# Kernel optimization log

Measured on AMD Instinct MI355X. Metric: run time of the kernel, lower is better.

Reference implementation:

```python
import jax, jax.numpy as jnp
import numpy as np

B, T, D, H = 32, 2048, 512, 512


def setup_inputs() -> dict:
    key = jax.random.key(0)
    ks = jax.random.split(key, 16)
    s_x = 1.0 / np.sqrt(D)
    s_h = 1.0 / np.sqrt(H)
    return {
        "x": jax.random.normal(ks[0], (B, T, D), dtype=jnp.float32),
        "Wxi": jax.random.normal(ks[1], (D, H), dtype=jnp.float32) * s_x,
        "Whi": jax.random.normal(ks[2], (H, H), dtype=jnp.float32) * s_h,
        "bi": jax.random.normal(ks[3], (H,), dtype=jnp.float32) * 0.01,
        "Wxf": jax.random.normal(ks[4], (D, H), dtype=jnp.float32) * s_x,
        "Whf": jax.random.normal(ks[5], (H, H), dtype=jnp.float32) * s_h,
        "bf": jax.random.normal(ks[6], (H,), dtype=jnp.float32) * 0.01,
        "Wxo": jax.random.normal(ks[7], (D, H), dtype=jnp.float32) * s_x,
        "Who": jax.random.normal(ks[8], (H, H), dtype=jnp.float32) * s_h,
        "bo": jax.random.normal(ks[9], (H,), dtype=jnp.float32) * 0.01,
        "Wxc": jax.random.normal(ks[10], (D, H), dtype=jnp.float32) * s_x,
        "Whc": jax.random.normal(ks[11], (H, H), dtype=jnp.float32) * s_h,
        "bc": jax.random.normal(ks[12], (H,), dtype=jnp.float32) * 0.01,
        "Wd": jax.random.normal(ks[13], (H, 1), dtype=jnp.float32) * s_h,
        "bd": jnp.zeros((1,), dtype=jnp.float32),
    }


def _lstm(x, Wxi, Whi, bi, Wxf, Whf, bf, Wxo, Who, bo, Wxc, Whc, bc):
    # Precompute input projections for all timesteps in one batched GEMM each.
    # Shapes: [B, T, H] -> transpose to time-major [T, B, H] for scan.
    xi = (jnp.einsum('btd,dh->bth', x, Wxi) + bi).transpose(1, 0, 2)
    xf = (jnp.einsum('btd,dh->bth', x, Wxf) + bf).transpose(1, 0, 2)
    xo = (jnp.einsum('btd,dh->bth', x, Wxo) + bo).transpose(1, 0, 2)
    xc = (jnp.einsum('btd,dh->bth', x, Wxc) + bc).transpose(1, 0, 2)

    h0 = jnp.zeros((x.shape[0], Whi.shape[0]), dtype=x.dtype)
    c0 = jnp.zeros_like(h0)

    def step(carry, gates_t):
        h, c = carry
        gi, gf, go, gc = gates_t
        I = jax.nn.sigmoid(gi + h @ Whi)
        F = jax.nn.sigmoid(gf + h @ Whf)
        O = jax.nn.sigmoid(go + h @ Who)
        Ct = jnp.tanh(gc + h @ Whc)
        c_new = F * c + I * Ct
        h_new = O * jnp.tanh(c_new)
        return (h_new, c_new), h_new

    _, hs = jax.lax.scan(step, (h0, c0), (xi, xf, xo, xc))
    return hs.transpose(1, 0, 2)  # [B, T, H]


def reference(x, Wxi, Whi, bi, Wxf, Whf, bf, Wxo, Who, bo, Wxc, Whc, bc, Wd, bd):
    hs = _lstm(x, Wxi, Whi, bi, Wxf, Whf, bf, Wxo, Who, bo, Wxc, Whc, bc)
    return jnp.einsum('bth,ho->bto', hs, Wd) + bd  # [B, T, 1]
```

## Files before the change

kernel.cpp:

```cpp
#include <hip/hip_runtime.h>
#include <cstdint>
#include <cstddef>

#define B_  32
#define T_  2048
#define D_  512
#define H_  512
#define NWG 32

typedef unsigned int   u32;
typedef unsigned short u16;
typedef u32   u32x4  __attribute__((ext_vector_type(4)));
typedef u32   u32x2  __attribute__((ext_vector_type(2)));
typedef float f32x4  __attribute__((ext_vector_type(4)));
typedef __bf16 bf16x8 __attribute__((ext_vector_type(8)));

__device__ __forceinline__ u16 f2bf(float f) {
  u32 u = __builtin_bit_cast(u32, f);
  u32 r = (u + 0x7fffu + ((u >> 16) & 1u)) >> 16;
  return (u16)r;
}
__device__ __forceinline__ f32x4 g4_from_bf(u32x2 p) {
  f32x4 r;
  r[0] = __builtin_bit_cast(float, (p[0] & 0xffffu) << 16);
  r[1] = __builtin_bit_cast(float, (p[0] & 0xffff0000u));
  r[2] = __builtin_bit_cast(float, (p[1] & 0xffffu) << 16);
  r[3] = __builtin_bit_cast(float, (p[1] & 0xffff0000u));
  return r;
}
__device__ __forceinline__ float sigm(float x) {
  return __builtin_amdgcn_rcpf(1.0f + __expf(-x));
}
__device__ __forceinline__ float tanh_fast(float x) {
  return 1.0f - 2.0f * __builtin_amdgcn_rcpf(__expf(2.0f * x) + 1.0f);
}

__global__ __launch_bounds__(256) void k_cast_x(const float* __restrict__ x,
                                                u16* __restrict__ xb) {
  long i = (long)blockIdx.x * 256 + threadIdx.x;
  int  dc = (int)(i & 63);
  long m  = i >> 6;
  int  t  = (int)(m >> 5), b = (int)(m & 31);
  const float* src = x + ((long)b * T_ + t) * D_ + (dc << 3);
  f32x4 a = *(const f32x4*)(src);
  f32x4 c = *(const f32x4*)(src + 4);
  u32x4 pv;
  pv[0] = (u32)f2bf(a[0]) | ((u32)f2bf(a[1]) << 16);
  pv[1] = (u32)f2bf(a[2]) | ((u32)f2bf(a[3]) << 16);
  pv[2] = (u32)f2bf(c[0]) | ((u32)f2bf(c[1]) << 16);
  pv[3] = (u32)f2bf(c[2]) | ((u32)f2bf(c[3]) << 16);
  *(u32x4*)(xb + (m << 9) + (dc << 3)) = pv;
}

__global__ __launch_bounds__(256) void k_pack_w(
    const float* __restrict__ Wxi, const float* __restrict__ Whi, const float* __restrict__ bi,
    const float* __restrict__ Wxf, const float* __restrict__ Whf, const float* __restrict__ bfv,
    const float* __restrict__ Wxo, const float* __restrict__ Who, const float* __restrict__ bo,
    const float* __restrict__ Wxc, const float* __restrict__ Whc, const float* __restrict__ bc,
    u16* __restrict__ w4xt, u16* __restrict__ w4ht, float* __restrict__ bias4) {
  int blk = blockIdx.x, tid = threadIdx.x;
  if (blk == 1024) {
    for (int i = tid; i < 2048; i += 256) {
      int hcol = i >> 2, g = i & 3;
      const float* bsrc = (g == 0 ? bi : g == 1 ? bfv : g == 2 ? bo : bc);
      bias4[i] = bsrc[hcol];
    }
    return;
  }
  bool isx = (blk < 512);
  long s = (long)(isx ? blk : blk - 512) * 256 + tid;
  int n = (int)(s >> 6);
  int c = (int)(s & 63);
  int hcol = n >> 2, g = n & 3;
  const float* W = isx ? (g == 0 ? Wxi : g == 1 ? Wxf : g == 2 ? Wxo : Wxc)
                       : (g == 0 ? Whi : g == 1 ? Whf : g == 2 ? Who : Whc);
  u16* dst = (isx ? w4xt : w4ht) + ((long)n << 9) + (c << 3);
#pragma unroll
  for (int j = 0; j < 8; j++) dst[j] = f2bf(W[(long)((c << 3) + j) * H_ + hcol]);
}

template <int G32>
__global__ __launch_bounds__(256) void k_gemm(const u16* __restrict__ xb,
                                              const u16* __restrict__ w4xt,
                                              const float* __restrict__ bias4,
                                              char* __restrict__ gates0) {
  __shared__ __align__(16) unsigned char As[128 * 32 * 2];
  __shared__ __align__(16) unsigned char Bs[128 * 32 * 2];
  int tid = threadIdx.x;
  int bm = blockIdx.x & 511;
  int bn = blockIdx.x >> 9;
  long m0 = (long)bm << 7;
  int  n0 = bn << 7;
  int wv = tid >> 6, lane = tid & 63;
  int wr = wv >> 1, wc = wv & 1;
  int lr = lane & 15, lc = lane >> 4;

  f32x4 acc[4][4];
#pragma unroll
  for (int i = 0; i < 4; i++)
#pragma unroll
    for (int j = 0; j < 4; j++) acc[i][j] = (f32x4){0.f, 0.f, 0.f, 0.f};

  for (int kt = 0; kt < 16; kt++) {
#pragma unroll
    for (int h = 0; h < 2; h++) {
      int s = h * 256 + tid;
      int row = s >> 2, ch = s & 3;
      u32x4 va = *(const u32x4*)(xb + ((m0 + row) << 9) + (kt << 5) + (ch << 3));
      *(u32x4*)(As + (((row << 6) + (ch << 4)) ^ ((row & 3) << 4))) = va;
      u32x4 vb = *(const u32x4*)(w4xt + (((long)n0 + row) << 9) + (kt << 5) + (ch << 3));
      *(u32x4*)(Bs + (((row << 6) + (ch << 4)) ^ ((row & 3) << 4))) = vb;
    }
    __syncthreads();
    bf16x8 af[4], bfr[4];
#pragma unroll
    for (int mi = 0; mi < 4; mi++) {
      int row = (wr << 6) + (mi << 4) + lr;
      af[mi] = __builtin_bit_cast(bf16x8,
          *(const u32x4*)(As + (((row << 6) + (lc << 4)) ^ ((row & 3) << 4))));
    }
#pragma unroll
    for (int ni = 0; ni < 4; ni++) {
      int row = (wc << 6) + (ni << 4) + lr;
      bfr[ni] = __builtin_bit_cast(bf16x8,
          *(const u32x4*)(Bs + (((row << 6) + (lc << 4)) ^ ((row & 3) << 4))));
    }
#pragma unroll
    for (int mi = 0; mi < 4; mi++)
#pragma unroll
      for (int ni = 0; ni < 4; ni++)
        acc[mi][ni] = __builtin_amdgcn_mfma_f32_16x16x32_bf16(af[mi], bfr[ni], acc[mi][ni], 0, 0, 0);
    __syncthreads();
  }
#pragma unroll
  for (int mi = 0; mi < 4; mi++) {
#pragma unroll
    for (int ni = 0; ni < 4; ni++) {
      int col = n0 + (wc << 6) + (ni << 4) + lr;
      float bias = bias4[col];
#pragma unroll
      for (int r = 0; r < 4; r++) {
        long row = m0 + (wr << 6) + (mi << 4) + (lc << 2) + r;
        float v = acc[mi][ni][r] + bias;
        if constexpr (G32) ((float*)gates0)[(row << 11) + col] = v;
        else               ((u16*)gates0)[(row << 11) + col] = f2bf(v);
      }
    }
  }
}

template <int G32>
__global__ __launch_bounds__(256, 1) void k_rnn(const u16* __restrict__ w4ht,
                                                const char* __restrict__ gates0,
                                                const float* __restrict__ wd,
                                                u16* __restrict__ h_buf,
                                                float* __restrict__ po,
                                                u32* __restrict__ flags) {
  __shared__ __align__(16) float G_all[32 * 64];
  __shared__ float hn_s[32 * 16];
  __shared__ float wd_s[16];

  const int tid = threadIdx.x;
  const int w = blockIdx.x;
  const int wv = tid >> 6, lane = tid & 63;
  const int lr = lane & 15, lc = lane >> 4;
  const int hhalf = wv >> 1;
  const int wcol  = wv & 1;
  const int ncol0 = (wcol << 5) + lr;
  const int ncol1 = ncol0 + 16;

  u32x4 wfr0[16], wfr1[16];
  {
    const u16* wb = w4ht + ((long)(w << 6) << 9);
#pragma unroll
    for (int kk = 0; kk < 16; kk++) {
      wfr0[kk] = *(const u32x4*)(wb + ((long)ncol0 << 9) + (kk << 5) + (lc << 3));
      wfr1[kk] = *(const u32x4*)(wb + ((long)ncol1 << 9) + (kk << 5) + (lc << 3));
    }
  }
  if (tid < 16) wd_s[tid] = wd[(w << 4) + tid];
  __syncthreads();

  const int pb = tid >> 4;
  const int jj = tid & 15;
  float c0 = 0.f, c1 = 0.f;

  const int arow = (hhalf << 4) + lr;
  const u32 hbase = (u32)(arow << 10);
  const u32 poll_off = (u32)((lane & 31) << 6);
  const u32 flag_off = (u32)(w << 6);
  const u32 st0 = (u32)((((pb) << 9) + (w << 4) + jj) << 1);
  const u32 st1 = (u32)((((pb + 16) << 9) + (w << 4) + jj) << 1);

#pragma unroll 1
  for (int t = 0; t < T_; t++) {
    const u16* hb_cur = h_buf + ((t & 1) << 14);
    u16* hb_nxt = h_buf + (((t + 1) & 1) << 14);

    f32x4 gfa, gfb; u32x2 gba, gbb;
    {
      long i0 = ((long)t * 32 + pb) * 2048 + (w << 6) + (jj << 2);
      long i1 = i0 + 16 * 2048;
      if constexpr (G32) {
        gfa = *(const f32x4*)((const float*)gates0 + i0);
        gfb = *(const f32x4*)((const float*)gates0 + i1);
      } else {
        gba = *(const u32x2*)((const u16*)gates0 + i0);
        gbb = *(const u32x2*)((const u16*)gates0 + i1);
      }
    }

    if (t > 0) {
      u32 fv;
      do {
        asm volatile("global_load_dword %0, %1, %2 sc1\n\ts_waitcnt vmcnt(0)"
                     : "=v"(fv) : "v"(poll_off), "s"(flags) : "memory");
      } while (!__all(fv >= (u32)t));
    }

    u32x4 ha[16];
#pragma unroll
    for (int kk = 0; kk < 16; kk++) {
      asm volatile("global_load_dwordx4 %0, %1, %2 sc1"
                   : "=v"(ha[kk]) : "v"(hbase + (u32)(kk << 6) + (u32)(lc << 4)),
                     "s"(hb_cur));
    }
    asm volatile("s_waitcnt vmcnt(0)" ::: "memory");
    __builtin_amdgcn_sched_barrier(0);

    f32x4 acc0 = {0.f, 0.f, 0.f, 0.f}, acc1 = {0.f, 0.f, 0.f, 0.f};
#pragma unroll
    for (int kk = 0; kk < 16; kk++) {
      bf16x8 a = __builtin_bit_cast(bf16x8, ha[kk]);
      acc0 = __builtin_amdgcn_mfma_f32_16x16x32_bf16(a, __builtin_bit_cast(bf16x8, wfr0[kk]), acc0, 0, 0, 0);
      acc1 = __builtin_amdgcn_mfma_f32_16x16x32_bf16(a, __builtin_bit_cast(bf16x8, wfr1[kk]), acc1, 0, 0, 0);
    }
#pragma unroll
    for (int r = 0; r < 4; r++) {
      int grow = (hhalf << 4) + (lc << 2) + r;
      G_all[(grow << 6) + ncol0] = acc0[r];
      G_all[(grow << 6) + ncol1] = acc1[r];
    }
    __syncthreads();

    {
      f32x4 g0a, g0b;
      if constexpr (G32) { g0a = gfa; g0b = gfb; }
      else { g0a = g4_from_bf(gba); g0b = g4_from_bf(gbb); }

      f32x4 gv = *(const f32x4*)(&G_all[(pb << 6) + (jj << 2)]);
      float I = sigm(gv[0] + g0a[0]);
      float F = sigm(gv[1] + g0a[1]);
      float O = sigm(gv[2] + g0a[2]);
      float Ct = tanh_fast(gv[3] + g0a[3]);
      float cn = F * c0 + I * Ct;
      float hn = O * tanh_fast(cn);
      c0 = cn;
      hn_s[(pb << 4) + jj] = hn;
      u32 hv0 = (u32)f2bf(hn);
      asm volatile("global_store_short %0, %1, %2 sc1"
                   :: "v"(st0), "v"(hv0), "s"(hb_nxt) : "memory");

      f32x4 gw = *(const f32x4*)(&G_all[((pb + 16) << 6) + (jj << 2)]);
      float I2 = sigm(gw[0] + g0b[0]);
      float F2 = sigm(gw[1] + g0b[1]);
      float O2 = sigm(gw[2] + g0b[2]);
      float Ct2 = tanh_fast(gw[3] + g0b[3]);
      float cn2 = F2 * c1 + I2 * Ct2;
      float hn2 = O2 * tanh_fast(cn2);
      c1 = cn2;
      hn_s[((pb + 16) << 4) + jj] = hn2;
      u32 hv1 = (u32)f2bf(hn2);
      asm volatile("global_store_short %0, %1, %2 sc1"
                   :: "v"(st1), "v"(hv1), "s"(hb_nxt) : "memory");
    }

    asm volatile("s_waitcnt vmcnt(0)" ::: "memory");
    __syncthreads();
    if (tid == 0) {
      u32 fval = (u32)(t + 1);
      asm volatile("global_store_dword %0, %1, %2 sc1"
                   :: "v"(flag_off), "v"(fval), "s"(flags) : "memory");
    }

    if (tid < 32) {
      float s = 0.f;
#pragma unroll
      for (int j = 0; j < 16; j++) s += hn_s[(tid << 4) + j] * wd_s[j];
      po[((long)t * NWG + w) * 32 + tid] = s;
    }
  }
}

__global__ __launch_bounds__(256) void k_reduce(const float* __restrict__ po,
                                                const float* __restrict__ bd,
                                                float* __restrict__ out) {
  int tid = threadIdx.x;
  int b = tid & 31, tl = tid >> 5;
  int t = blockIdx.x * 8 + tl;
  float s = bd[0];
#pragma unroll
  for (int w = 0; w < NWG; w++) s += po[((long)t * NWG + w) * 32 + b];
  out[(long)b * T_ + t] = s;
}

extern "C" void kernel_launch(void* const* d_in, const int* in_sizes, int n_in,
                              void* d_out, int out_size, void* d_ws, size_t ws_size,
                              hipStream_t stream) {
  const float* x   = (const float*)d_in[0];
  const float* Wxi = (const float*)d_in[1];
  const float* Whi = (const float*)d_in[2];
  const float* bi  = (const float*)d_in[3];
  const float* Wxf = (const float*)d_in[4];
  const float* Whf = (const float*)d_in[5];
  const float* bfv = (const float*)d_in[6];
  const float* Wxo = (const float*)d_in[7];
  const float* Who = (const float*)d_in[8];
  const float* bo  = (const float*)d_in[9];
  const float* Wxc = (const float*)d_in[10];
  const float* Whc = (const float*)d_in[11];
  const float* bc  = (const float*)d_in[12];
  const float* Wd  = (const float*)d_in[13];
  const float* bd  = (const float*)d_in[14];

  char* ws = (char*)d_ws;
  constexpr size_t OFF_FLAGS = 0;
  constexpr size_t OFF_HBUF  = 2048;
  constexpr size_t OFF_PO    = OFF_HBUF + 65536;
  constexpr size_t OFF_XB    = OFF_PO + 8388608;
  constexpr size_t OFF_W4XT  = OFF_XB + 67108864;
  constexpr size_t OFF_W4HT  = OFF_W4XT + 2097152;
  constexpr size_t OFF_BIAS  = OFF_W4HT + 2097152;
  constexpr size_t OFF_G0    = OFF_BIAS + 8192;
  constexpr size_t TOT_F32   = OFF_G0 + (size_t)65536 * 2048 * 4;
  bool g32 = (ws_size >= TOT_F32);

  u32* flags     = (u32*)(ws + OFF_FLAGS);
  u16* h_buf     = (u16*)(ws + OFF_HBUF);
  float* po      = (float*)(ws + OFF_PO);
  u16* xb        = (u16*)(ws + OFF_XB);
  u16* w4xt      = (u16*)(ws + OFF_W4XT);
  u16* w4ht      = (u16*)(ws + OFF_W4HT);
  float* bias4   = (float*)(ws + OFF_BIAS);
  char* gates0   = ws + OFF_G0;

  hipMemsetAsync(d_ws, 0, OFF_PO, stream);

  k_cast_x<<<16384, 256, 0, stream>>>(x, xb);
  k_pack_w<<<1025, 256, 0, stream>>>(Wxi, Whi, bi, Wxf, Whf, bfv, Wxo, Who, bo,
                                     Wxc, Whc, bc, w4xt, w4ht, bias4);
  if (g32) {
    k_gemm<1><<<8192, 256, 0, stream>>>(xb, w4xt, bias4, gates0);
    k_rnn<1><<<NWG, 256, 0, stream>>>(w4ht, gates0, Wd, h_buf, po, flags);
  } else {
    k_gemm<0><<<8192, 256, 0, stream>>>(xb, w4xt, bias4, gates0);
    k_rnn<0><<<NWG, 256, 0, stream>>>(w4ht, gates0, Wd, h_buf, po, flags);
  }
  k_reduce<<<256, 256, 0, stream>>>(po, bd, (float*)d_out);
}
```

Baseline: 9.061 ms.

## Remove per-step block barriers: per-wave flags, LDS weights, prefetched gate inputs

The recurrent kernel now stages each workgroup's slice of the recurrent weights in swizzled LDS. Each wave computes all 32 batch rows for its own 4 hidden columns, so gates stay in registers and the per-step LDS exchange and both __syncthreads disappear. Each wave publishes its own flag, pollers read two flags per lane, the next step's input gates are prefetched during the current step, and the output dot-product partials are reduced with shuffles into a four-times-larger partial buffer. This targets the intra-block barrier latency on the serial critical path, at the cost of 128 flags to poll, extra LDS weight reads per step, and a larger final reduction.

Measured after the change: 17.41 ms. 1.92x slower.

```diff
diff --git a/kernel.cpp b/kernel.cpp
--- a/kernel.cpp
+++ b/kernel.cpp
@@ -156,139 +156,169 @@
                                                 u16* __restrict__ h_buf,
                                                 float* __restrict__ po,
                                                 u32* __restrict__ flags) {
-  __shared__ __align__(16) float G_all[32 * 64];
-  __shared__ float hn_s[32 * 16];
-  __shared__ float wd_s[16];
+  __shared__ __align__(16) unsigned char whs[64 * 1024];
 
   const int tid = threadIdx.x;
   const int w = blockIdx.x;
   const int wv = tid >> 6, lane = tid & 63;
   const int lr = lane & 15, lc = lane >> 4;
-  const int hhalf = wv >> 1;
-  const int wcol  = wv & 1;
-  const int ncol0 = (wcol << 5) + lr;
-  const int ncol1 = ncol0 + 16;
-
-  u32x4 wfr0[16], wfr1[16];
-  {
-    const u16* wb = w4ht + ((long)(w << 6) << 9);
-#pragma unroll
-    for (int kk = 0; kk < 16; kk++) {
-      wfr0[kk] = *(const u32x4*)(wb + ((long)ncol0 << 9) + (kk << 5) + (lc << 3));
-      wfr1[kk] = *(const u32x4*)(wb + ((long)ncol1 << 9) + (kk << 5) + (lc << 3));
-    }
-  }
-  if (tid < 16) wd_s[tid] = wd[(w << 4) + tid];
+
+#pragma unroll 4
+  for (int i = 0; i < 16; i++) {
+    int s = i * 256 + tid;
+    int n = s >> 6, c = s & 63;
+    u32x4 v = *(const u32x4*)(w4ht + ((long)((w << 6) + n) << 9) + (c << 3));
+    *(u32x4*)(whs + (((n << 10) + (c << 4)) ^ ((n & 7) << 4))) = v;
+  }
   __syncthreads();
 
-  const int pb = tid >> 4;
-  const int jj = tid & 15;
+  const int mycol = (w << 4) + (wv << 2) + lc;
+  const float wdr = wd[mycol];
   float c0 = 0.f, c1 = 0.f;
 
-  const int arow = (hhalf << 4) + lr;
-  const u32 hbase = (u32)(arow << 10);
-  const u32 poll_off = (u32)((lane & 31) << 6);
-  const u32 flag_off = (u32)(w << 6);
-  const u32 st0 = (u32)((((pb) << 9) + (w << 4) + jj) << 1);
-  const u32 st1 = (u32)((((pb + 16) << 9) + (w << 4) + jj) << 1);
+  const u32 hoff = (u32)((lr << 10) + (lc << 4));
+  const u32 st0 = (u32)(((lr << 9) + mycol) << 1);
+  const u32 st1 = (u32)((((lr + 16) << 9) + mycol) << 1);
+  const u32 poll_off = (u32)(lane << 3);
+  const u32 flag_off = (u32)(((w << 2) + wv) << 2);
+
+  const int sh = G32 ? 2 : 1;
+  u32 go = (u32)(((lr << 11) + (mycol << 2)) << sh);
+  const u32 gstep = 65536u << sh;
+  const u32 gdel  = 32768u << sh;
+
+  u32x4 gfa, gfb, gna, gnb;
+  u32x2 g2a, g2b, g2na, g2nb;
+  if constexpr (G32) {
+    asm volatile("global_load_dwordx4 %0, %1, %2" : "=v"(gfa) : "v"(go), "s"(gates0));
+    asm volatile("global_load_dwordx4 %0, %1, %2" : "=v"(gfb) : "v"(go + gdel), "s"(gates0));
+  } else {
+    asm volatile("global_load_dwordx2 %0, %1, %2" : "=v"(g2a) : "v"(go), "s"(gates0));
+    asm volatile("global_load_dwordx2 %0, %1, %2" : "=v"(g2b) : "v"(go + gdel), "s"(gates0));
+  }
+
+  const u32 wrow  = (u32)((wv << 4) + lr);
+  const u32 wbase = wrow << 10;
+  const u32 wswz  = (wrow & 7) << 4;
 
 #pragma unroll 1
   for (int t = 0; t < T_; t++) {
     const u16* hb_cur = h_buf + ((t & 1) << 14);
     u16* hb_nxt = h_buf + (((t + 1) & 1) << 14);
 
-    f32x4 gfa, gfb; u32x2 gba, gbb;
-    {
-      long i0 = ((long)t * 32 + pb) * 2048 + (w << 6) + (jj << 2);
-      long i1 = i0 + 16 * 2048;
-      if constexpr (G32) {
-        gfa = *(const f32x4*)((const float*)gates0 + i0);
-        gfb = *(const f32x4*)((const float*)gates0 + i1);
-      } else {
-        gba = *(const u32x2*)((const u16*)gates0 + i0);
-        gbb = *(const u32x2*)((const u16*)gates0 + i1);
-      }
-    }
-
     if (t > 0) {
-      u32 fv;
+      u32x2 fv;
       do {
-        asm volatile("global_load_dword %0, %1, %2 sc1\n\ts_waitcnt vmcnt(0)"
+        asm volatile("global_load_dwordx2 %0, %1, %2 sc1\n\ts_waitcnt vmcnt(0)"
                      : "=v"(fv) : "v"(poll_off), "s"(flags) : "memory");
-      } while (!__all(fv >= (u32)t));
-    }
-
-    u32x4 ha[16];
+      } while (!__all((fv[0] >= (u32)t) && (fv[1] >= (u32)t)));
+    }
+
+    u32x4 hlo[16], hhi[16];
 #pragma unroll
     for (int kk = 0; kk < 16; kk++) {
       asm volatile("global_load_dwordx4 %0, %1, %2 sc1"
-                   : "=v"(ha[kk]) : "v"(hbase + (u32)(kk << 6) + (u32)(lc << 4)),
-                     "s"(hb_cur));
+                   : "=v"(hlo[kk]) : "v"(hoff + (u32)(kk << 6)), "s"(hb_cur));
+      asm volatile("global_load_dwordx4 %0, %1, %2 sc1"
+                   : "=v"(hhi[kk]) : "v"(hoff + (u32)(kk << 6) + 16384u), "s"(hb_cur));
+    }
+
+    f32x4 aL0 = {0.f,0.f,0.f,0.f}, aL1 = {0.f,0.f,0.f,0.f};
+    f32x4 aH0 = {0.f,0.f,0.f,0.f}, aH1 = {0.f,0.f,0.f,0.f};
+    asm volatile("s_waitcnt vmcnt(16)" ::: "memory");
+    __builtin_amdgcn_sched_barrier(0);
+#pragma unroll
+    for (int kk = 0; kk < 8; kk++) {
+      bf16x8 aw = __builtin_bit_cast(bf16x8,
+          *(const u32x4*)(whs + ((wbase + (u32)((kk << 6) + (lc << 4))) ^ wswz)));
+      bf16x8 bl = __builtin_bit_cast(bf16x8, hlo[kk]);
+      bf16x8 bh = __builtin_bit_cast(bf16x8, hhi[kk]);
+      if (kk & 1) {
+        aL1 = __builtin_amdgcn_mfma_f32_16x16x32_bf16(aw, bl, aL1, 0, 0, 0);
+        aH1 = __builtin_amdgcn_mfma_f32_16x16x32_bf16(aw, bh, aH1, 0, 0, 0);
+      } else {
+        aL0 = __builtin_amdgcn_mfma_f32_16x16x32_bf16(aw, bl, aL0, 0, 0, 0);
+        aH0 = __builtin_amdgcn_mfma_f32_16x16x32_bf16(aw, bh, aH0, 0, 0, 0);
+      }
     }
     asm volatile("s_waitcnt vmcnt(0)" ::: "memory");
     __builtin_amdgcn_sched_barrier(0);
-
-    f32x4 acc0 = {0.f, 0.f, 0.f, 0.f}, acc1 = {0.f, 0.f, 0.f, 0.f};
-#pragma unroll
-    for (int kk = 0; kk < 16; kk++) {
-      bf16x8 a = __builtin_bit_cast(bf16x8, ha[kk]);
-      acc0 = __builtin_amdgcn_mfma_f32_16x16x32_bf16(a, __builtin_bit_cast(bf16x8, wfr0[kk]), acc0, 0, 0, 0);
-      acc1 = __builtin_amdgcn_mfma_f32_16x16x32_bf16(a, __builtin_bit_cast(bf16x8, wfr1[kk]), acc1, 0, 0, 0);
-    }
-#pragma unroll
-    for (int r = 0; r < 4; r++) {
-      int grow = (hhalf << 4) + (lc << 2) + r;
-      G_all[(grow << 6) + ncol0] = acc0[r];
-      G_all[(grow << 6) + ncol1] = acc1[r];
-    }
-    __syncthreads();
-
-    {
-      f32x4 g0a, g0b;
-      if constexpr (G32) { g0a = gfa; g0b = gfb; }
-      else { g0a = g4_from_bf(gba); g0b = g4_from_bf(gbb); }
-
-      f32x4 gv = *(const f32x4*)(&G_all[(pb << 6) + (jj << 2)]);
-      float I = sigm(gv[0] + g0a[0]);
-      float F = sigm(gv[1] + g0a[1]);
-      float O = sigm(gv[2] + g0a[2]);
-      float Ct = tanh_fast(gv[3] + g0a[3]);
-      float cn = F * c0 + I * Ct;
-      float hn = O * tanh_fast(cn);
-      c0 = cn;
-      hn_s[(pb << 4) + jj] = hn;
-      u32 hv0 = (u32)f2bf(hn);
-      asm volatile("global_store_short %0, %1, %2 sc1"
-                   :: "v"(st0), "v"(hv0), "s"(hb_nxt) : "memory");
-
-      f32x4 gw = *(const f32x4*)(&G_all[((pb + 16) << 6) + (jj << 2)]);
-      float I2 = sigm(gw[0] + g0b[0]);
-      float F2 = sigm(gw[1] + g0b[1]);
-      float O2 = sigm(gw[2] + g0b[2]);
-      float Ct2 = tanh_fast(gw[3] + g0b[3]);
-      float cn2 = F2 * c1 + I2 * Ct2;
-      float hn2 = O2 * tanh_fast(cn2);
-      c1 = cn2;
-      hn_s[((pb + 16) << 4) + jj] = hn2;
-      u32 hv1 = (u32)f2bf(hn2);
-      asm volatile("global_store_short %0, %1, %2 sc1"
-                   :: "v"(st1), "v"(hv1), "s"(hb_nxt) : "memory");
-    }
-
-    asm volatile("s_waitcnt vmcnt(0)" ::: "memory");
-    __syncthreads();
-    if (tid == 0) {
+#pragma unroll
+    for (int kk = 8; kk < 16; kk++) {
+      bf16x8 aw = __builtin_bit_cast(bf16x8,
+          *(const u32x4*)(whs + ((wbase + (u32)((kk << 6) + (lc << 4))) ^ wswz)));
+      bf16x8 bl = __builtin_bit_cast(bf16x8, hlo[kk]);
+      bf16x8 bh = __builtin_bit_cast(bf16x8, hhi[kk]);
+      if (kk & 1) {
+        aL1 = __builtin_amdgcn_mfma_f32_16x16x32_bf16(aw, bl, aL1, 0, 0, 0);
+        aH1 = __builtin_amdgcn_mfma_f32_16x16x32_bf16(aw, bh, aH1, 0, 0, 0);
+      } else {
+        aL0 = __builtin_amdgcn_mfma_f32_16x16x32_bf16(aw, bl, aL0, 0, 0, 0);
+        aH0 = __builtin_amdgcn_mfma_f32_16x16x32_bf16(aw, bh, aH0, 0, 0, 0);
+      }
+    }
+    f32x4 GL = aL0 + aL1, GH = aH0 + aH1;
+
+    f32x4 g0a, g0b;
+    if constexpr (G32) {
+      g0a = __builtin_bit_cast(f32x4, gfa);
+      g0b = __builtin_bit_cast(f32x4, gfb);
+    } else {
+      g0a = g4_from_bf(g2a);
+      g0b = g4_from_bf(g2b);
+    }
+
+    float I  = sigm(GL[0] + g0a[0]);
+    float F  = sigm(GL[1] + g0a[1]);
+    float O  = sigm(GL[2] + g0a[2]);
+    float Ct = tanh_fast(GL[3] + g0a[3]);
+    float cn = F * c0 + I * Ct;
+    float hn = O * tanh_fast(cn);
+    c0 = cn;
+    u32 hv0 = (u32)f2bf(hn);
+    asm volatile("global_store_short %0, %1, %2 sc1"
+                 :: "v"(st0), "v"(hv0), "s"(hb_nxt) : "memory");
+
+    float I2  = sigm(GH[0] + g0b[0]);
+    float F2  = sigm(GH[1] + g0b[1]);
+    float O2  = sigm(GH[2] + g0b[2]);
+    float Ct2 = tanh_fast(GH[3] + g0b[3]);
+    float cn2 = F2 * c1 + I2 * Ct2;
+    float hn2 = O2 * tanh_fast(cn2);
+    c1 = cn2;
+    u32 hv1 = (u32)f2bf(hn2);
+    asm volatile("global_store_short %0, %1, %2 sc1"
+                 :: "v"(st1), "v"(hv1), "s"(hb_nxt) : "memory");
+
+    u32 gq = (t + 1 < T_) ? (go + gstep) : go;
+    if constexpr (G32) {
+      asm volatile("global_load_dwordx4 %0, %1, %2" : "=v"(gna) : "v"(gq), "s"(gates0));
+      asm volatile("global_load_dwordx4 %0, %1, %2" : "=v"(gnb) : "v"(gq + gdel), "s"(gates0));
+    } else {
+      asm volatile("global_load_dwordx2 %0, %1, %2" : "=v"(g2na) : "v"(gq), "s"(gates0));
+      asm volatile("global_load_dwordx2 %0, %1, %2" : "=v"(g2nb) : "v"(gq + gdel), "s"(gates0));
+    }
+    go = gq;
+
+    asm volatile("s_waitcnt vmcnt(2)" ::: "memory");
+    __builtin_amdgcn_sched_barrier(0);
+    if (lane == 0) {
       u32 fval = (u32)(t + 1);
       asm volatile("global_store_dword %0, %1, %2 sc1"
                    :: "v"(flag_off), "v"(fval), "s"(flags) : "memory");
     }
 
-    if (tid < 32) {
-      float s = 0.f;
-#pragma unroll
-      for (int j = 0; j < 16; j++) s += hn_s[(tid << 4) + j] * wd_s[j];
-      po[((long)t * NWG + w) * 32 + tid] = s;
-    }
+    float p0 = hn * wdr, p1 = hn2 * wdr;
+    p0 += __shfl_xor(p0, 16); p0 += __shfl_xor(p0, 32);
+    p1 += __shfl_xor(p1, 16); p1 += __shfl_xor(p1, 32);
+    if (lc == 0) {
+      float* pp = po + ((long)t * 128 + (w << 2) + wv) * 32;
+      pp[lr] = p0;
+      pp[lr + 16] = p1;
+    }
+
+    if constexpr (G32) { gfa = gna; gfb = gnb; }
+    else               { g2a = g2na; g2b = g2nb; }
   }
 }
 
@@ -299,8 +329,8 @@
   int b = tid & 31, tl = tid >> 5;
   int t = blockIdx.x * 8 + tl;
   float s = bd[0];
-#pragma unroll
-  for (int w = 0; w < NWG; w++) s += po[((long)t * NWG + w) * 32 + b];
+#pragma unroll 8
+  for (int w = 0; w < 128; w++) s += po[((long)t * 128 + w) * 32 + b];
   out[(long)b * T_ + t] = s;
 }
 
@@ -325,9 +355,9 @@
 
   char* ws = (char*)d_ws;
   constexpr size_t OFF_FLAGS = 0;
-  constexpr size_t OFF_HBUF  = 2048;
+  constexpr size_t OFF_HBUF  = 1024;
   constexpr size_t OFF_PO    = OFF_HBUF + 65536;
-  constexpr size_t OFF_XB    = OFF_PO + 8388608;
+  constexpr size_t OFF_XB    = OFF_PO + 33554432;
   constexpr size_t OFF_W4XT  = OFF_XB + 67108864;
   constexpr size_t OFF_W4HT  = OFF_W4XT + 2097152;
   constexpr size_t OFF_BIAS  = OFF_W4HT + 2097152;
@@ -344,7 +374,7 @@
   float* bias4   = (float*)(ws + OFF_BIAS);
   char* gates0   = ws + OFF_G0;
 
-  hipMemsetAsync(d_ws, 0, OFF_PO, stream);
+  hipMemsetAsync(d_ws, 0, OFF_HBUF + 65536, stream);
 
   k_cast_x<<<16384, 256, 0, stream>>>(x, xb);
   k_pack_w<<<1025, 256, 0, stream>>>(Wxi, Whi, bi, Wxf, Whf, bfv, Wxo, Who, bo,
```

## Move recurrent weights to swizzled LDS, use per-wave flags and shuffle-reduce output

Applied to the files above, without the earlier changes.

The recurrent weight fragments now live in a 64KB XOR-swizzled LDS buffer instead of 32 u32x4 registers per thread, which frees VGPRs at the cost of two LDS reads per MFMA. The end-of-step __syncthreads before publishing the flag is removed: each wave writes its own flag, and wave 0 polls all 128 per-wave flags with dwordx2 loads before a block barrier. The dense-output partial dot product moves from a 32-thread LDS loop to a shuffle-xor reduction across the 16 lanes. Together these target the per-step barrier and serial tail latency in the persistent recurrent loop, but add LDS traffic on the critical path and a wider flag poll.

Result: slower. 11.36 ms (+25.3%).

```diff
diff --git a/kernel.cpp b/kernel.cpp
--- a/kernel.cpp
+++ b/kernel.cpp
@@ -156,9 +156,8 @@
                                                 u16* __restrict__ h_buf,
                                                 float* __restrict__ po,
                                                 u32* __restrict__ flags) {
+  __shared__ __align__(16) unsigned char whs[64 * 1024];
   __shared__ __align__(16) float G_all[32 * 64];
-  __shared__ float hn_s[32 * 16];
-  __shared__ float wd_s[16];
 
   const int tid = threadIdx.x;
   const int w = blockIdx.x;
@@ -169,33 +168,43 @@
   const int ncol0 = (wcol << 5) + lr;
   const int ncol1 = ncol0 + 16;
 
-  u32x4 wfr0[16], wfr1[16];
-  {
-    const u16* wb = w4ht + ((long)(w << 6) << 9);
-#pragma unroll
-    for (int kk = 0; kk < 16; kk++) {
-      wfr0[kk] = *(const u32x4*)(wb + ((long)ncol0 << 9) + (kk << 5) + (lc << 3));
-      wfr1[kk] = *(const u32x4*)(wb + ((long)ncol1 << 9) + (kk << 5) + (lc << 3));
-    }
-  }
-  if (tid < 16) wd_s[tid] = wd[(w << 4) + tid];
+#pragma unroll 4
+  for (int i = 0; i < 16; i++) {
+    int s = i * 256 + tid;
+    int n = s >> 6, c = s & 63;
+    u32x4 v = *(const u32x4*)(w4ht + ((long)((w << 6) + n) << 9) + (c << 3));
+    *(u32x4*)(whs + (((n << 10) + (c << 4)) ^ ((n & 7) << 4))) = v;
+  }
   __syncthreads();
 
   const int pb = tid >> 4;
   const int jj = tid & 15;
   float c0 = 0.f, c1 = 0.f;
-
-  const int arow = (hhalf << 4) + lr;
-  const u32 hbase = (u32)(arow << 10);
-  const u32 poll_off = (u32)((lane & 31) << 6);
-  const u32 flag_off = (u32)(w << 6);
+  const float wdr = wd[(w << 4) + jj];
+
+  const u32 hbase = (u32)(((hhalf << 4) + lr) << 10);
+  const u32 poll_off = (u32)(lane << 3);
+  const u32 flag_off = (u32)(((w << 2) + wv) << 2);
   const u32 st0 = (u32)((((pb) << 9) + (w << 4) + jj) << 1);
   const u32 st1 = (u32)((((pb + 16) << 9) + (w << 4) + jj) << 1);
+  const u32 b0base = (u32)(ncol0 << 10), b0swz = (u32)((ncol0 & 7) << 4);
+  const u32 b1base = (u32)(ncol1 << 10), b1swz = (u32)((ncol1 & 7) << 4);
 
 #pragma unroll 1
   for (int t = 0; t < T_; t++) {
     const u16* hb_cur = h_buf + ((t & 1) << 14);
     u16* hb_nxt = h_buf + (((t + 1) & 1) << 14);
+
+    if (t > 0) {
+      if (wv == 0) {
+        u32x2 fv;
+        do {
+          asm volatile("global_load_dwordx2 %0, %1, %2 sc1\n\ts_waitcnt vmcnt(0)"
+                       : "=v"(fv) : "v"(poll_off), "s"(flags) : "memory");
+        } while (!__all((fv[0] >= (u32)t) && (fv[1] >= (u32)t)));
+      }
+      __syncthreads();
+    }
 
     f32x4 gfa, gfb; u32x2 gba, gbb;
     {
@@ -210,14 +219,6 @@
       }
     }
 
-    if (t > 0) {
-      u32 fv;
-      do {
-        asm volatile("global_load_dword %0, %1, %2 sc1\n\ts_waitcnt vmcnt(0)"
-                     : "=v"(fv) : "v"(poll_off), "s"(flags) : "memory");
-      } while (!__all(fv >= (u32)t));
-    }
-
     u32x4 ha[16];
 #pragma unroll
     for (int kk = 0; kk < 16; kk++) {
@@ -228,12 +229,15 @@
     asm volatile("s_waitcnt vmcnt(0)" ::: "memory");
     __builtin_amdgcn_sched_barrier(0);
 
-    f32x4 acc0 = {0.f, 0.f, 0.f, 0.f}, acc1 = {0.f, 0.f, 0.f, 0.f};
+    f32x4 acc0 = {0.f,0.f,0.f,0.f}, acc1 = {0.f,0.f,0.f,0.f};
 #pragma unroll
     for (int kk = 0; kk < 16; kk++) {
-      bf16x8 a = __builtin_bit_cast(bf16x8, ha[kk]);
-      acc0 = __builtin_amdgcn_mfma_f32_16x16x32_bf16(a, __builtin_bit_cast(bf16x8, wfr0[kk]), acc0, 0, 0, 0);
-      acc1 = __builtin_amdgcn_mfma_f32_16x16x32_bf16(a, __builtin_bit_cast(bf16x8, wfr1[kk]), acc1, 0, 0, 0);
+      u32 ko = (u32)((kk << 6) + (lc << 4));
+      bf16x8 a  = __builtin_bit_cast(bf16x8, ha[kk]);
+      bf16x8 b0 = __builtin_bit_cast(bf16x8, *(const u32x4*)(whs + ((b0base + ko) ^ b0swz)));
+      bf16x8 b1 = __builtin_bit_cast(bf16x8, *(const u32x4*)(whs + ((b1base + ko) ^ b1swz)));
+      acc0 = __builtin_amdgcn_mfma_f32_16x16x32_bf16(a, b0, acc0, 0, 0, 0);
+      acc1 = __builtin_amdgcn_mfma_f32_16x16x32_bf16(a, b1, acc1, 0, 0, 0);
     }
 #pragma unroll
     for (int r = 0; r < 4; r++) {
@@ -243,6 +247,7 @@
     }
     __syncthreads();
 
+    float hnA, hnB;
     {
       f32x4 g0a, g0b;
       if constexpr (G32) { g0a = gfa; g0b = gfb; }
@@ -254,10 +259,9 @@
       float O = sigm(gv[2] + g0a[2]);
       float Ct = tanh_fast(gv[3] + g0a[3]);
       float cn = F * c0 + I * Ct;
-      float hn = O * tanh_fast(cn);
+      hnA = O * tanh_fast(cn);
       c0 = cn;
-      hn_s[(pb << 4) + jj] = hn;
-      u32 hv0 = (u32)f2bf(hn);
+      u32 hv0 = (u32)f2bf(hnA);
       asm volatile("global_store_short %0, %1, %2 sc1"
                    :: "v"(st0), "v"(hv0), "s"(hb_nxt) : "memory");
 
@@ -267,27 +271,30 @@
       float O2 = sigm(gw[2] + g0b[2]);
       float Ct2 = tanh_fast(gw[3] + g0b[3]);
       float cn2 = F2 * c1 + I2 * Ct2;
-      float hn2 = O2 * tanh_fast(cn2);
+      hnB = O2 * tanh_fast(cn2);
       c1 = cn2;
-      hn_s[((pb + 16) << 4) + jj] = hn2;
-      u32 hv1 = (u32)f2bf(hn2);
+      u32 hv1 = (u32)f2bf(hnB);
       asm volatile("global_store_short %0, %1, %2 sc1"
                    :: "v"(st1), "v"(hv1), "s"(hb_nxt) : "memory");
     }
 
     asm volatile("s_waitcnt vmcnt(0)" ::: "memory");
-    __syncthreads();
-    if (tid == 0) {
+    __builtin_amdgcn_sched_barrier(0);
+    if (lane == 0) {
       u32 fval = (u32)(t + 1);
       asm volatile("global_store_dword %0, %1, %2 sc1"
                    :: "v"(flag_off), "v"(fval), "s"(flags) : "memory");
     }
 
-    if (tid < 32) {
-      float s = 0.f;
-#pragma unroll
-      for (int j = 0; j < 16; j++) s += hn_s[(tid << 4) + j] * wd_s[j];
-      po[((long)t * NWG + w) * 32 + tid] = s;
+    float pA = hnA * wdr, pB = hnB * wdr;
+    pA += __shfl_xor(pA, 1); pA += __shfl_xor(pA, 2);
+    pA += __shfl_xor(pA, 4); pA += __shfl_xor(pA, 8);
+    pB += __shfl_xor(pB, 1); pB += __shfl_xor(pB, 2);
+    pB += __shfl_xor(pB, 4); pB += __shfl_xor(pB, 8);
+    if (jj == 0) {
+      float* pp = po + ((long)t * NWG + w) * 32;
+      pp[pb] = pA;
+      pp[pb + 16] = pB;
     }
   }
 }
```

## Prefetch flag poll early and compute output projection with wave shuffles

Applied to the files above, without the earlier changes.

Issues the flag load for the next step right after publishing this step's flag, so the poll latency overlaps the output-projection work. On the next iteration the spin loop is skipped if the prefetched value already meets the target. The output dot product with Wd now uses in-register xor-shuffle reductions instead of a shared-memory staging array read by 32 threads, removing the hn_s/wd_s LDS traffic and one setup barrier. The prefetched flag can still be stale, in which case the old polling path runs as a fallback.

After: 9.170 ms. About the same (+1.2%).

```diff
diff --git a/kernel.cpp b/kernel.cpp
--- a/kernel.cpp
+++ b/kernel.cpp
@@ -157,8 +157,6 @@
                                                 float* __restrict__ po,
                                                 u32* __restrict__ flags) {
   __shared__ __align__(16) float G_all[32 * 64];
-  __shared__ float hn_s[32 * 16];
-  __shared__ float wd_s[16];
 
   const int tid = threadIdx.x;
   const int w = blockIdx.x;
@@ -178,12 +176,11 @@
       wfr1[kk] = *(const u32x4*)(wb + ((long)ncol1 << 9) + (kk << 5) + (lc << 3));
     }
   }
-  if (tid < 16) wd_s[tid] = wd[(w << 4) + tid];
-  __syncthreads();
 
   const int pb = tid >> 4;
   const int jj = tid & 15;
   float c0 = 0.f, c1 = 0.f;
+  const float wdr = wd[(w << 4) + jj];
 
   const int arow = (hhalf << 4) + lr;
   const u32 hbase = (u32)(arow << 10);
@@ -191,6 +188,8 @@
   const u32 flag_off = (u32)(w << 6);
   const u32 st0 = (u32)((((pb) << 9) + (w << 4) + jj) << 1);
   const u32 st1 = (u32)((((pb + 16) << 9) + (w << 4) + jj) << 1);
+
+  u32 fpre = 0;
 
 #pragma unroll 1
   for (int t = 0; t < T_; t++) {
@@ -211,11 +210,14 @@
     }
 
     if (t > 0) {
-      u32 fv;
-      do {
-        asm volatile("global_load_dword %0, %1, %2 sc1\n\ts_waitcnt vmcnt(0)"
-                     : "=v"(fv) : "v"(poll_off), "s"(flags) : "memory");
-      } while (!__all(fv >= (u32)t));
+      asm volatile("s_waitcnt vmcnt(0)" ::: "memory");
+      if (!__all(fpre >= (u32)t)) {
+        u32 fv;
+        do {
+          asm volatile("global_load_dword %0, %1, %2 sc1\n\ts_waitcnt vmcnt(0)"
+                       : "=v"(fv) : "v"(poll_off), "s"(flags) : "memory");
+        } while (!__all(fv >= (u32)t));
+      }
     }
 
     u32x4 ha[16];
@@ -243,6 +245,7 @@
     }
     __syncthreads();
 
+    float hnA, hnB;
     {
       f32x4 g0a, g0b;
       if constexpr (G32) { g0a = gfa; g0b = gfb; }
@@ -254,10 +257,9 @@
       float O = sigm(gv[2] + g0a[2]);
       float Ct = tanh_fast(gv[3] + g0a[3]);
       float cn = F * c0 + I * Ct;
-      float hn = O * tanh_fast(cn);
+      hnA = O * tanh_fast(cn);
       c0 = cn;
-      hn_s[(pb << 4) + jj] = hn;
-      u32 hv0 = (u32)f2bf(hn);
+      u32 hv0 = (u32)f2bf(hnA);
       asm volatile("global_store_short %0, %1, %2 sc1"
                    :: "v"(st0), "v"(hv0), "s"(hb_nxt) : "memory");
 
@@ -267,10 +269,9 @@
       float O2 = sigm(gw[2] + g0b[2]);
       float Ct2 = tanh_fast(gw[3] + g0b[3]);
       float cn2 = F2 * c1 + I2 * Ct2;
-      float hn2 = O2 * tanh_fast(cn2);
+      hnB = O2 * tanh_fast(cn2);
       c1 = cn2;
-      hn_s[((pb + 16) << 4) + jj] = hn2;
-      u32 hv1 = (u32)f2bf(hn2);
+      u32 hv1 = (u32)f2bf(hnB);
       asm volatile("global_store_short %0, %1, %2 sc1"
                    :: "v"(st1), "v"(hv1), "s"(hb_nxt) : "memory");
     }
@@ -283,11 +284,18 @@
                    :: "v"(flag_off), "v"(fval), "s"(flags) : "memory");
     }
 
-    if (tid < 32) {
-      float s = 0.f;
-#pragma unroll
-      for (int j = 0; j < 16; j++) s += hn_s[(tid << 4) + j] * wd_s[j];
-      po[((long)t * NWG + w) * 32 + tid] = s;
+    asm volatile("global_load_dword %0, %1, %2 sc1"
+                 : "=v"(fpre) : "v"(poll_off), "s"(flags));
+
+    float pA = hnA * wdr, pB = hnB * wdr;
+    pA += __shfl_xor(pA, 1); pA += __shfl_xor(pA, 2);
+    pA += __shfl_xor(pA, 4); pA += __shfl_xor(pA, 8);
+    pB += __shfl_xor(pB, 1); pB += __shfl_xor(pB, 2);
+    pB += __shfl_xor(pB, 4); pB += __shfl_xor(pB, 8);
+    if (jj == 0) {
+      float* pp = po + ((long)t * NWG + w) * 32;
+      pp[pb] = pA;
+      pp[pb + 16] = pB;
     }
   }
 }
```
